# Kernel optimization log

Hardware: AMD Instinct MI355X
Metric: run time of the kernel (lower is better)

## Reference

```python
import jax, jax.numpy as jnp
import numpy as np

N_QUBITS = 4


def _apply_rx(state, theta, wire):
    # state: [B, 2,2,2,2] complex64, theta: [B] real angles; RX on `wire`.
    st = jnp.moveaxis(state, wire + 1, -1)
    bshape = (theta.shape[0],) + (1,) * (st.ndim - 2)
    c = jnp.cos(theta * 0.5).reshape(bshape).astype(jnp.complex64)
    s = (-1j) * jnp.sin(theta * 0.5).reshape(bshape).astype(jnp.complex64)
    new = jnp.stack([c * st[..., 0] + s * st[..., 1],
                     s * st[..., 0] + c * st[..., 1]], axis=-1)
    return jnp.moveaxis(new, -1, wire + 1)


def _apply_cnot(state, control, target):
    st = jnp.moveaxis(state, (control + 1, target + 1), (-2, -1))
    new = jnp.stack([st[..., 0, :], st[..., 1, ::-1]], axis=-2)
    return jnp.moveaxis(new, (-2, -1), (control + 1, target + 1))


def _quantum_gate(angles, thetas):
    # angles: [B, n] data-encoding RX angles; thetas: [n] trainable RX angles.
    B, n = angles.shape
    state = jnp.zeros((B,) + (2,) * n, jnp.complex64)
    state = state.at[(slice(None),) + (0,) * n].set(1.0)  # |0...0>
    for w in range(n):
        state = _apply_rx(state, angles[:, w], w)
    for w in range(n):
        state = _apply_rx(state, jnp.broadcast_to(thetas[w], (B,)), w)
    for w in range(n):
        state = _apply_cnot(state, w, (w + 1) % n)
    probs = jnp.abs(state.reshape(B, 2 ** n)) ** 2  # [B, 16]
    bits = (np.arange(2 ** n)[:, None] >> np.arange(n - 1, -1, -1)[None, :]) & 1
    signs = jnp.asarray(1.0 - 2.0 * bits, jnp.float32)  # [16, n] PauliZ eigvals
    return probs @ signs  # [B, n] <Z_w> expectations


def setup_inputs() -> dict:
    key = jax.random.key(0)
    ks = jax.random.split(key, 12)
    B, D, H, n = 131072, 256, 4, N_QUBITS
    fan_in = D + H
    sc = 1.0 / np.sqrt(fan_in)
    inp = {
        'x': jax.random.normal(ks[0], (B, D), jnp.float32),
        'hx': jax.random.normal(ks[1], (B, H), jnp.float32),
        'cx': jax.random.normal(ks[2], (B, H), jnp.float32),
        'W_f': jax.random.normal(ks[3], (n, fan_in), jnp.float32) * sc,
        'b_f': jnp.zeros((n,), jnp.float32),
        'W_i': jax.random.normal(ks[4], (n, fan_in), jnp.float32) * sc,
        'b_i': jnp.zeros((n,), jnp.float32),
        'W_u': jax.random.normal(ks[5], (n, fan_in), jnp.float32) * sc,
        'b_u': jnp.zeros((n,), jnp.float32),
        'W_o': jax.random.normal(ks[6], (n, fan_in), jnp.float32) * sc,
        'b_o': jnp.zeros((n,), jnp.float32),
        'th_f': jax.random.normal(ks[7], (n,), jnp.float32),
        'th_i': jax.random.normal(ks[8], (n,), jnp.float32),
        'th_u': jax.random.normal(ks[9], (n,), jnp.float32),
        'th_o': jax.random.normal(ks[10], (n,), jnp.float32),
    }
    return inp


def reference(x, hx, cx, W_f, b_f, W_i, b_i, W_u, b_u, W_o, b_o,
              th_f, th_i, th_u, th_o):
    comb = jnp.concatenate([x, hx], axis=1)  # [B, D+H]
    f = jax.nn.sigmoid(_quantum_gate(comb @ W_f.T + b_f, th_f))
    i = jax.nn.sigmoid(_quantum_gate(comb @ W_i.T + b_i, th_i))
    g = jnp.tanh(_quantum_gate(comb @ W_u.T + b_u, th_u))
    o = jax.nn.sigmoid(_quantum_gate(comb @ W_o.T + b_o, th_o))
    c_new = f * cx + i * g
    h_new = o * jnp.tanh(c_new)
    return (h_new, c_new)
```

## Files before the change

kernel.cpp:

```cpp
#include <hip/hip_runtime.h>

#define NB    131072
#define TPB   128
#define FANIN 260

__device__ __forceinline__ float sigm_(float x) { return 1.0f / (1.0f + __expf(-x)); }
__device__ __forceinline__ float tanh_(float x) { return 1.0f - 2.0f / (__expf(2.0f * x) + 1.0f); }

__global__ void qlstm_prep(const float* __restrict__ Wf, const float* __restrict__ bf,
                           const float* __restrict__ Wi, const float* __restrict__ bi,
                           const float* __restrict__ Wu, const float* __restrict__ bu,
                           const float* __restrict__ Wo, const float* __restrict__ bo,
                           const float* __restrict__ thf, const float* __restrict__ thi,
                           const float* __restrict__ thu, const float* __restrict__ tho,
                           float* __restrict__ Wp, float* __restrict__ bth) {
    int t = blockIdx.x * blockDim.x + threadIdx.x;
    if (t < FANIN * 16) {
        int k = t >> 4, gw = t & 15, g = gw >> 2, w = gw & 3;
        const float* Wg = (g == 0) ? Wf : (g == 1) ? Wi : (g == 2) ? Wu : Wo;
        Wp[t] = Wg[w * FANIN + k];
    }
    if (t < 16) {
        int g = t >> 2, w = t & 3;
        const float* bg = (g == 0) ? bf  : (g == 1) ? bi  : (g == 2) ? bu  : bo;
        const float* tg = (g == 0) ? thf : (g == 1) ? thi : (g == 2) ? thu : tho;
        bth[t] = bg[w] + tg[w];
    }
}

__device__ __forceinline__ void consume8(const float4 (&b)[8],
                                         const float* __restrict__ wb,
                                         float (&acc)[16]) {
#pragma unroll
    for (int u = 0; u < 8; ++u) {
#pragma unroll
        for (int m = 0; m < 4; ++m) {
            float xe = (m == 0) ? b[u].x : (m == 1) ? b[u].y
                     : (m == 2) ? b[u].z : b[u].w;
            const float* wp = wb + (u * 4 + m) * 16;
#pragma unroll
            for (int j = 0; j < 16; ++j) acc[j] = fmaf(xe, wp[j], acc[j]);
        }
    }
}

__global__ __launch_bounds__(TPB, 4) void qlstm_main(
        const float* __restrict__ x, const float* __restrict__ hx,
        const float* __restrict__ cx, const float* __restrict__ Wp,
        const float* __restrict__ bth, float* __restrict__ out) {
    __shared__ float accx[64 * 16];

    const int tid  = threadIdx.x;
    const int lane = tid & 63;
    const int wv   = tid >> 6;
    const int wvu  = __builtin_amdgcn_readfirstlane(wv);
    const int row0 = blockIdx.x * 64;
    const int row  = row0 + lane;

    const float4* xr = (const float4*)x + (size_t)row * 64 + wvu * 32;
    const float*  wW = Wp + wvu * (4 * 512);

    float4 hv = make_float4(0.f, 0.f, 0.f, 0.f);
    float4 cxv = make_float4(0.f, 0.f, 0.f, 0.f);
    if (wvu == 1) hv  = ((const float4*)hx)[row];
    else          cxv = ((const float4*)cx)[row];

    float acc[16];
#pragma unroll
    for (int j = 0; j < 16; ++j) acc[j] = 0.0f;

    float4 A[8], B[8];
#pragma unroll
    for (int u = 0; u < 8; ++u) A[u] = xr[u];
#pragma unroll
    for (int u = 0; u < 8; ++u) B[u] = xr[8 + u];
    consume8(A, wW + 0 * 512, acc);
#pragma unroll
    for (int u = 0; u < 8; ++u) A[u] = xr[16 + u];
    consume8(B, wW + 1 * 512, acc);
#pragma unroll
    for (int u = 0; u < 8; ++u) B[u] = xr[24 + u];
    consume8(A, wW + 2 * 512, acc);
    consume8(B, wW + 3 * 512, acc);

    if (wvu == 1) {
        const float* wp = Wp + 256 * 16;
#pragma unroll
        for (int j = 0; j < 16; ++j) acc[j] = fmaf(hv.x, wp[j],      acc[j]);
#pragma unroll
        for (int j = 0; j < 16; ++j) acc[j] = fmaf(hv.y, wp[16 + j], acc[j]);
#pragma unroll
        for (int j = 0; j < 16; ++j) acc[j] = fmaf(hv.z, wp[32 + j], acc[j]);
#pragma unroll
        for (int j = 0; j < 16; ++j) acc[j] = fmaf(hv.w, wp[48 + j], acc[j]);
#pragma unroll
        for (int j4 = 0; j4 < 4; ++j4)
            ((float4*)accx)[lane * 4 + j4] =
                make_float4(acc[j4 * 4 + 0], acc[j4 * 4 + 1],
                            acc[j4 * 4 + 2], acc[j4 * 4 + 3]);
    }
    __syncthreads();
    if (wvu == 0) {
#pragma unroll
        for (int j4 = 0; j4 < 4; ++j4) {
            float4 p = ((const float4*)accx)[lane * 4 + j4];
            acc[j4 * 4 + 0] += p.x;
            acc[j4 * 4 + 1] += p.y;
            acc[j4 * 4 + 2] += p.z;
            acc[j4 * 4 + 3] += p.w;
        }

        float co[16];
#pragma unroll
        for (int j = 0; j < 16; ++j) co[j] = __cosf(acc[j] + bth[j]);

        float G[16];
#pragma unroll
        for (int g = 0; g < 4; ++g) {
            float c0 = co[g * 4 + 0], c1 = co[g * 4 + 1];
            float c2 = co[g * 4 + 2], c3 = co[g * 4 + 3];
            float e1 = c0 * c1;
            float e2 = e1 * c2;
            float e3 = e2 * c3;
            float e0 = c1 * c2 * c3;
            G[g * 4 + 0] = e0; G[g * 4 + 1] = e1; G[g * 4 + 2] = e2; G[g * 4 + 3] = e3;
        }

        float cxa[4] = {cxv.x, cxv.y, cxv.z, cxv.w};
        float hn[4], cn[4];
#pragma unroll
        for (int w = 0; w < 4; ++w) {
            float fg = sigm_(G[0 * 4 + w]);
            float ig = sigm_(G[1 * 4 + w]);
            float ug = tanh_(G[2 * 4 + w]);
            float og = sigm_(G[3 * 4 + w]);
            float c_ = fg * cxa[w] + ig * ug;
            cn[w] = c_;
            hn[w] = og * tanh_(c_);
        }

        ((float4*)out)[row]      = make_float4(hn[0], hn[1], hn[2], hn[3]);
        ((float4*)out)[NB + row] = make_float4(cn[0], cn[1], cn[2], cn[3]);
    }
}

extern "C" void kernel_launch(void* const* d_in, const int* in_sizes, int n_in,
                              void* d_out, int out_size, void* d_ws, size_t ws_size,
                              hipStream_t stream) {
    const float* x   = (const float*)d_in[0];
    const float* hx  = (const float*)d_in[1];
    const float* cx  = (const float*)d_in[2];
    const float* Wf  = (const float*)d_in[3];
    const float* bf  = (const float*)d_in[4];
    const float* Wi  = (const float*)d_in[5];
    const float* bi  = (const float*)d_in[6];
    const float* Wu  = (const float*)d_in[7];
    const float* bu  = (const float*)d_in[8];
    const float* Wo  = (const float*)d_in[9];
    const float* bo  = (const float*)d_in[10];
    const float* thf = (const float*)d_in[11];
    const float* thi = (const float*)d_in[12];
    const float* thu = (const float*)d_in[13];
    const float* tho = (const float*)d_in[14];

    float* Wp  = (float*)d_ws;
    float* bth = Wp + FANIN * 16;

    qlstm_prep<<<(FANIN * 16 + 255) / 256, 256, 0, stream>>>(
        Wf, bf, Wi, bi, Wu, bu, Wo, bo, thf, thi, thu, tho, Wp, bth);

    qlstm_main<<<NB / 64, TPB, 0, stream>>>(
        x, hx, cx, Wp, bth, (float*)d_out);
}
```

Baseline: 228.2 us.

## Split each row's reduction across four waves instead of two

Each block now runs four waves per 64 rows, and each wave handles a quarter of the 256 input columns. All 16 float4 loads are issued up front rather than in double-buffered halves. The three partial sums are combined through a larger, lane-contiguous shared buffer laid out to avoid bank conflicts. This gives more waves for latency hiding and a shorter serial FMA chain per thread, at the cost of more shared-memory traffic and a larger register footprint per thread.

```diff
diff --git a/kernel.cpp b/kernel.cpp
--- a/kernel.cpp
+++ b/kernel.cpp
@@ -1,7 +1,7 @@
 #include <hip/hip_runtime.h>
 
 #define NB    131072
-#define TPB   128
+#define TPB   256
 #define FANIN 260
 
 __device__ __forceinline__ float sigm_(float x) { return 1.0f / (1.0f + __expf(-x)); }
@@ -28,27 +28,11 @@
     }
 }
 
-__device__ __forceinline__ void consume8(const float4 (&b)[8],
-                                         const float* __restrict__ wb,
-                                         float (&acc)[16]) {
-#pragma unroll
-    for (int u = 0; u < 8; ++u) {
-#pragma unroll
-        for (int m = 0; m < 4; ++m) {
-            float xe = (m == 0) ? b[u].x : (m == 1) ? b[u].y
-                     : (m == 2) ? b[u].z : b[u].w;
-            const float* wp = wb + (u * 4 + m) * 16;
-#pragma unroll
-            for (int j = 0; j < 16; ++j) acc[j] = fmaf(xe, wp[j], acc[j]);
-        }
-    }
-}
-
 __global__ __launch_bounds__(TPB, 4) void qlstm_main(
         const float* __restrict__ x, const float* __restrict__ hx,
         const float* __restrict__ cx, const float* __restrict__ Wp,
         const float* __restrict__ bth, float* __restrict__ out) {
-    __shared__ float accx[64 * 16];
+    __shared__ float accx[16 * 3 * 64];
 
     const int tid  = threadIdx.x;
     const int lane = tid & 63;
@@ -57,33 +41,35 @@
     const int row0 = blockIdx.x * 64;
     const int row  = row0 + lane;
 
-    const float4* xr = (const float4*)x + (size_t)row * 64 + wvu * 32;
-    const float*  wW = Wp + wvu * (4 * 512);
+    const float4* xr = (const float4*)x + (size_t)row * 64 + wvu * 16;
 
-    float4 hv = make_float4(0.f, 0.f, 0.f, 0.f);
+    float4 xb[16];
+#pragma unroll
+    for (int u = 0; u < 16; ++u) xb[u] = xr[u];
+
+    float4 hv  = make_float4(0.f, 0.f, 0.f, 0.f);
     float4 cxv = make_float4(0.f, 0.f, 0.f, 0.f);
-    if (wvu == 1) hv  = ((const float4*)hx)[row];
-    else          cxv = ((const float4*)cx)[row];
+    if (wvu == 3) hv  = ((const float4*)hx)[row];
+    if (wvu == 0) cxv = ((const float4*)cx)[row];
 
     float acc[16];
 #pragma unroll
     for (int j = 0; j < 16; ++j) acc[j] = 0.0f;
 
-    float4 A[8], B[8];
+    const float* wbase = Wp + wvu * 64 * 16;
 #pragma unroll
-    for (int u = 0; u < 8; ++u) A[u] = xr[u];
+    for (int c4 = 0; c4 < 16; ++c4) {
 #pragma unroll
-    for (int u = 0; u < 8; ++u) B[u] = xr[8 + u];
-    consume8(A, wW + 0 * 512, acc);
+        for (int m = 0; m < 4; ++m) {
+            float xe = (m == 0) ? xb[c4].x : (m == 1) ? xb[c4].y
+                     : (m == 2) ? xb[c4].z : xb[c4].w;
+            const float* wp = wbase + (c4 * 4 + m) * 16;
 #pragma unroll
-    for (int u = 0; u < 8; ++u) A[u] = xr[16 + u];
-    consume8(B, wW + 1 * 512, acc);
-#pragma unroll
-    for (int u = 0; u < 8; ++u) B[u] = xr[24 + u];
-    consume8(A, wW + 2 * 512, acc);
-    consume8(B, wW + 3 * 512, acc);
+            for (int j = 0; j < 16; ++j) acc[j] = fmaf(xe, wp[j], acc[j]);
+        }
+    }
 
-    if (wvu == 1) {
+    if (wvu == 3) {
         const float* wp = Wp + 256 * 16;
 #pragma unroll
         for (int j = 0; j < 16; ++j) acc[j] = fmaf(hv.x, wp[j],      acc[j]);
@@ -93,22 +79,21 @@
         for (int j = 0; j < 16; ++j) acc[j] = fmaf(hv.z, wp[32 + j], acc[j]);
 #pragma unroll
         for (int j = 0; j < 16; ++j) acc[j] = fmaf(hv.w, wp[48 + j], acc[j]);
+    }
+
+    if (wvu != 0) {
 #pragma unroll
-        for (int j4 = 0; j4 < 4; ++j4)
-            ((float4*)accx)[lane * 4 + j4] =
-                make_float4(acc[j4 * 4 + 0], acc[j4 * 4 + 1],
-                            acc[j4 * 4 + 2], acc[j4 * 4 + 3]);
+        for (int j = 0; j < 16; ++j)
+            accx[(j * 3 + (wvu - 1)) * 64 + lane] = acc[j];
     }
     __syncthreads();
+
     if (wvu == 0) {
 #pragma unroll
-        for (int j4 = 0; j4 < 4; ++j4) {
-            float4 p = ((const float4*)accx)[lane * 4 + j4];
-            acc[j4 * 4 + 0] += p.x;
-            acc[j4 * 4 + 1] += p.y;
-            acc[j4 * 4 + 2] += p.z;
-            acc[j4 * 4 + 3] += p.w;
-        }
+        for (int j = 0; j < 16; ++j)
+            acc[j] += accx[(j * 3 + 0) * 64 + lane]
+                    + accx[(j * 3 + 1) * 64 + lane]
+                    + accx[(j * 3 + 2) * 64 + lane];
 
         float co[16];
 #pragma unroll
```

After: 223.5 us. 1.02x faster.
